# Performance work log

Hardware: AMD Instinct MI355X
Metric: run time of the kernel (lower is better)

Reference implementation:

```python
import jax, jax.numpy as jnp
import numpy as np

D_MODEL = 1024
NUM_HEADS = 16
HEAD_DIM = D_MODEL // NUM_HEADS
B, S = 4, 2048


def setup_inputs() -> dict:
    key = jax.random.key(0)
    ks = jax.random.split(key, 11)
    scale = 1.0 / np.sqrt(D_MODEL)
    return {
        "query": jax.random.normal(ks[0], (B, S, D_MODEL), jnp.float32),
        "key": jax.random.normal(ks[1], (B, S, D_MODEL), jnp.float32),
        "value": jax.random.normal(ks[2], (B, S, D_MODEL), jnp.float32),
        "Wq": jax.random.normal(ks[3], (D_MODEL, D_MODEL), jnp.float32) * scale,
        "bq": jnp.zeros((D_MODEL,), jnp.float32),
        "Wk": jax.random.normal(ks[4], (D_MODEL, D_MODEL), jnp.float32) * scale,
        "bk": jnp.zeros((D_MODEL,), jnp.float32),
        "Wv": jax.random.normal(ks[5], (D_MODEL, D_MODEL), jnp.float32) * scale,
        "bv": jnp.zeros((D_MODEL,), jnp.float32),
        "Wo": jax.random.normal(ks[6], (D_MODEL, D_MODEL), jnp.float32) * scale,
        "bo": jnp.zeros((D_MODEL,), jnp.float32),
    }


def reference(query, key, value, Wq, bq, Wk, bk, Wv, bv, Wo, bo):
    b = query.shape[0]
    # nn.Linear: x @ W.T + b; weights stored [out, in]
    def split_heads(x):
        return x.reshape(b, -1, NUM_HEADS, HEAD_DIM).transpose(0, 2, 1, 3)  # [b,h,s,d]
    q = split_heads(query @ Wq.T + bq)
    k = split_heads(key @ Wk.T + bk)
    v = split_heads(value @ Wv.T + bv)
    scores = jnp.einsum("bhqd,bhkd->bhqk", q, k) / np.sqrt(HEAD_DIM)
    weights = jax.nn.softmax(scores, axis=-1)
    out = jnp.einsum("bhqk,bhkd->bhqd", weights, v)
    out = out.transpose(0, 2, 1, 3).reshape(b, -1, D_MODEL)
    return out @ Wo.T + bo
```

## Files before the change

kernel.cpp:

```cpp
#include <hip/hip_runtime.h>

typedef __bf16 bf16;
typedef __bf16 bf16x4 __attribute__((ext_vector_type(4)));
typedef __bf16 bf16x8 __attribute__((ext_vector_type(8)));
typedef float f32x4 __attribute__((ext_vector_type(4)));

#define MFMA16(a, b, c) __builtin_amdgcn_mfma_f32_16x16x32_bf16((a), (b), (c), 0, 0, 0)

#define QSCALE 0.1803368808f

__device__ __forceinline__ void async_cp16(const bf16* g, bf16* l) {
    __builtin_amdgcn_global_load_lds((const __attribute__((address_space(1))) void*)g,
                                     (__attribute__((address_space(3))) void*)l, 16, 0, 0);
}

__global__ void cvt_bf16(const float* __restrict__ x, bf16* __restrict__ y, int n8) {
    int i = blockIdx.x * 256 + threadIdx.x;
    if (i >= n8) return;
    const float4* p = (const float4*)(x + (size_t)i * 8);
    float4 a = p[0], c = p[1];
    bf16x8 o;
    o[0] = (bf16)a.x; o[1] = (bf16)a.y; o[2] = (bf16)a.z; o[3] = (bf16)a.w;
    o[4] = (bf16)c.x; o[5] = (bf16)c.y; o[6] = (bf16)c.z; o[7] = (bf16)c.w;
    *(bf16x8*)(y + (size_t)i * 8) = o;
}

__device__ __forceinline__ void gemm_core(
    const bf16* __restrict__ A, const bf16* __restrict__ W,
    const float* __restrict__ bias, void* __restrict__ Cout,
    int mode, int m0, int n0)
{
    __shared__ bf16 As[128 * 32];
    __shared__ bf16 Bs[128 * 32];
    const int K = 1024;
    const int tid = threadIdx.x;
    const int lane = tid & 63, wave = tid >> 6;
    const int l15 = lane & 15, quad = lane >> 4;
    const int wm = wave >> 1, wn = wave & 1;

    f32x4 acc[4][4] = {};

    const int r0 = tid >> 2, k8 = (tid & 3) * 8;
    const bf16* Ag0 = A + (size_t)(m0 + r0) * K + k8;
    const bf16* Ag1 = A + (size_t)(m0 + r0 + 64) * K + k8;
    const bf16* Wg0 = W + (size_t)(n0 + r0) * K + k8;
    const bf16* Wg1 = W + (size_t)(n0 + r0 + 64) * K + k8;
    bf16* Al0 = As + tid * 8;
    bf16* Al1 = As + (tid + 256) * 8;
    bf16* Bl0 = Bs + tid * 8;
    bf16* Bl1 = Bs + (tid + 256) * 8;

    for (int k0 = 0; k0 < K; k0 += 32) {
        __syncthreads();
        async_cp16(Ag0 + k0, Al0);
        async_cp16(Ag1 + k0, Al1);
        async_cp16(Wg0 + k0, Bl0);
        async_cp16(Wg1 + k0, Bl1);
        __syncthreads();

        bf16x8 af[4], bfr[4];
#pragma unroll
        for (int t = 0; t < 4; ++t) {
            af[t]  = *(const bf16x8*)(As + (wm * 64 + t * 16 + l15) * 32 + quad * 8);
            bfr[t] = *(const bf16x8*)(Bs + (wn * 64 + t * 16 + l15) * 32 + quad * 8);
        }
#pragma unroll
        for (int mt = 0; mt < 4; ++mt)
#pragma unroll
            for (int nt = 0; nt < 4; ++nt)
                acc[mt][nt] = MFMA16(af[mt], bfr[nt], acc[mt][nt]);
    }

#pragma unroll
    for (int mt = 0; mt < 4; ++mt) {
#pragma unroll
        for (int nt = 0; nt < 4; ++nt) {
            int col = n0 + wn * 64 + nt * 16 + l15;
            float bcol = (mode == 2) ? 0.0f : bias[col];
#pragma unroll
            for (int r = 0; r < 4; ++r) {
                int row = m0 + wm * 64 + mt * 16 + quad * 4 + r;
                float val = acc[mt][nt][r];
                if (mode == 2) {
                    val += bias[row];
                    int bb = col >> 11, s = col & 2047;
                    int u = s & 63;
                    int sp = (s & ~63) | (((u & 15) << 2) | (u >> 4));
                    ((bf16*)Cout)[((size_t)(bb * 1024 + row) << 11) + sp] = (bf16)val;
                } else if (mode == 3) {
                    ((float*)Cout)[(size_t)row * 1024 + col] = val + bcol;
                } else {
                    val += bcol;
                    if (mode == 0) val *= QSCALE;
                    int bb = row >> 11, s = row & 2047, hh = col >> 6, d = col & 63;
                    ((bf16*)Cout)[(((size_t)(bb * 16 + hh) * 2048 + s) << 6) + d] = (bf16)val;
                }
            }
        }
    }
}

struct QkvArgs {
    const bf16* A[3];
    const bf16* W[3];
    const float* bias[3];
    bf16* out[3];
};

__global__ __launch_bounds__(256) void qkv_gemm(QkvArgs t) {
    int z = blockIdx.y;
    int bx = blockIdx.x;
    int m0, n0;
    if (z < 2) { m0 = (bx & 63) * 128; n0 = (bx >> 6) * 128; }
    else       { m0 = (bx & 7) * 128;  n0 = (bx >> 3) * 128; }
    gemm_core(t.A[z], t.W[z], t.bias[z], t.out[z], z, m0, n0);
}

__global__ __launch_bounds__(256) void oproj_gemm(
    const bf16* __restrict__ A, const bf16* __restrict__ W,
    const float* __restrict__ bias, float* __restrict__ Cout) {
    gemm_core(A, W, bias, Cout, 3, blockIdx.x * 128, blockIdx.y * 128);
}

__global__ __launch_bounds__(128, 2) void attn_kernel(
    const bf16* __restrict__ Qh, const bf16* __restrict__ Kh,
    const bf16* __restrict__ Vtg, bf16* __restrict__ AO)
{
    __shared__ bf16 Kl[64 * 64];
    __shared__ bf16 Vl[64 * 64];
    __shared__ bf16 Pl[2][64 * 72];

    const int tid = threadIdx.x;
    const int lane = tid & 63, wave = tid >> 6;
    const int l15 = lane & 15, quad = lane >> 4;
    const int l7 = l15 & 7;
    const int h = blockIdx.y, b = blockIdx.z;
    const int bh = b * 16 + h;
    const size_t base = (size_t)bh << 17;
    const int q0 = blockIdx.x * 128 + wave * 64;

    bf16x8 qf[4][2];
#pragma unroll
    for (int mt = 0; mt < 4; ++mt)
#pragma unroll
        for (int ks = 0; ks < 2; ++ks)
            qf[mt][ks] = *(const bf16x8*)(Qh + base + (q0 + mt * 16 + l15) * 64 + ks * 32 + quad * 8);

    f32x4 o[4][4] = {};
    float ls[4][4] = {};

    int srow[4], scol[4];
#pragma unroll
    for (int i = 0; i < 4; ++i) {
        int s = tid + i * 128;
        srow[i] = s >> 3;
        scol[i] = ((s & 7) ^ (srow[i] & 7)) * 8;
    }
    bf16* Pw = Pl[wave];

    for (int kt = 0; kt < 2048; kt += 64) {
        __syncthreads();
#pragma unroll
        for (int i = 0; i < 4; ++i) {
            int s = tid + i * 128;
            async_cp16(Kh + base + (size_t)(kt + srow[i]) * 64 + scol[i], Kl + s * 8);
            async_cp16(Vtg + base + (size_t)srow[i] * 2048 + kt + scol[i], Vl + s * 8);
        }
        __syncthreads();

        bf16x8 kb[2][4];
#pragma unroll
        for (int ks = 0; ks < 2; ++ks)
#pragma unroll
            for (int nt = 0; nt < 4; ++nt)
                kb[ks][nt] = *(const bf16x8*)(Kl + (nt * 16 + l15) * 64 + (((ks * 4 + quad) ^ l7) * 8));

#pragma unroll
        for (int mt = 0; mt < 4; ++mt) {
            f32x4 sc[4] = {};
#pragma unroll
            for (int ks = 0; ks < 2; ++ks)
#pragma unroll
                for (int nt = 0; nt < 4; ++nt)
                    sc[nt] = MFMA16(qf[mt][ks], kb[ks][nt], sc[nt]);
#pragma unroll
            for (int r = 0; r < 4; ++r) {
                float p0 = __builtin_amdgcn_exp2f(sc[0][r]);
                float p1 = __builtin_amdgcn_exp2f(sc[1][r]);
                float p2 = __builtin_amdgcn_exp2f(sc[2][r]);
                float p3 = __builtin_amdgcn_exp2f(sc[3][r]);
                ls[mt][r] += (p0 + p1) + (p2 + p3);
                bf16x4 pk = {(bf16)p0, (bf16)p1, (bf16)p2, (bf16)p3};
                *(bf16x4*)(Pw + (mt * 16 + quad * 4 + r) * 72 + l15 * 4) = pk;
            }
        }

        bf16x8 vb[2][4];
#pragma unroll
        for (int ks = 0; ks < 2; ++ks)
#pragma unroll
            for (int nt = 0; nt < 4; ++nt)
                vb[ks][nt] = *(const bf16x8*)(Vl + (nt * 16 + l15) * 64 + (((ks * 4 + quad) ^ l7) * 8));
#pragma unroll
        for (int mt = 0; mt < 4; ++mt)
#pragma unroll
            for (int ks = 0; ks < 2; ++ks) {
                bf16x8 pa = *(const bf16x8*)(Pw + (mt * 16 + l15) * 72 + ks * 32 + quad * 8);
#pragma unroll
                for (int nt = 0; nt < 4; ++nt)
                    o[mt][nt] = MFMA16(pa, vb[ks][nt], o[mt][nt]);
            }
    }

#pragma unroll
    for (int mt = 0; mt < 4; ++mt)
#pragma unroll
        for (int r = 0; r < 4; ++r) {
            float l = ls[mt][r];
            l += __shfl_xor(l, 1, 64);
            l += __shfl_xor(l, 2, 64);
            l += __shfl_xor(l, 4, 64);
            l += __shfl_xor(l, 8, 64);
            float inv = 1.0f / l;
            int s = q0 + mt * 16 + quad * 4 + r;
            size_t rowbase = ((size_t)(b * 2048 + s)) * 1024 + h * 64;
#pragma unroll
            for (int nt = 0; nt < 4; ++nt)
                AO[rowbase + nt * 16 + l15] = (bf16)(o[mt][nt][r] * inv);
        }
}

extern "C" void kernel_launch(void* const* d_in, const int* in_sizes, int n_in,
                              void* d_out, int out_size, void* d_ws, size_t ws_size,
                              hipStream_t stream) {
    const float* q  = (const float*)d_in[0];
    const float* k  = (const float*)d_in[1];
    const float* v  = (const float*)d_in[2];
    const float* Wq = (const float*)d_in[3];
    const float* bq = (const float*)d_in[4];
    const float* Wk = (const float*)d_in[5];
    const float* bk = (const float*)d_in[6];
    const float* Wv = (const float*)d_in[7];
    const float* bv = (const float*)d_in[8];
    const float* Wo = (const float*)d_in[9];
    const float* bo = (const float*)d_in[10];
    float* out = (float*)d_out;

    const size_t NX = (size_t)8192 * 1024;
    const size_t NW = (size_t)1024 * 1024;
    bf16* ws  = (bf16*)d_ws;
    bf16* Xq  = ws;
    bf16* Xk  = Xq + NX;
    bf16* Xv  = Xk + NX;
    bf16* Wqb = Xv + NX;
    bf16* Wkb = Wqb + NW;
    bf16* Wvb = Wkb + NW;
    bf16* Wob = Wvb + NW;
    bf16* Qh  = Wob + NW;
    bf16* Kh  = Qh + NX;
    bf16* Vt  = Kh + NX;
    bf16* AO  = Xq;

    int nx8 = (int)(NX / 8), nw8 = (int)(NW / 8);
    cvt_bf16<<<nx8 / 256, 256, 0, stream>>>(q, Xq, nx8);
    cvt_bf16<<<nx8 / 256, 256, 0, stream>>>(k, Xk, nx8);
    cvt_bf16<<<nx8 / 256, 256, 0, stream>>>(v, Xv, nx8);
    cvt_bf16<<<nw8 / 256, 256, 0, stream>>>(Wq, Wqb, nw8);
    cvt_bf16<<<nw8 / 256, 256, 0, stream>>>(Wk, Wkb, nw8);
    cvt_bf16<<<nw8 / 256, 256, 0, stream>>>(Wv, Wvb, nw8);
    cvt_bf16<<<nw8 / 256, 256, 0, stream>>>(Wo, Wob, nw8);

    dim3 bb(256, 1, 1);
    QkvArgs t;
    t.A[0] = Xq;  t.W[0] = Wqb; t.bias[0] = bq; t.out[0] = Qh;
    t.A[1] = Xk;  t.W[1] = Wkb; t.bias[1] = bk; t.out[1] = Kh;
    t.A[2] = Wvb; t.W[2] = Xv;  t.bias[2] = bv; t.out[2] = Vt;
    qkv_gemm<<<dim3(512, 3), bb, 0, stream>>>(t);

    attn_kernel<<<dim3(16, 16, 4), dim3(128, 1, 1), 0, stream>>>(Qh, Kh, Vt, AO);

    oproj_gemm<<<dim3(64, 8), bb, 0, stream>>>(AO, Wob, bo, out);
}
```

Baseline: 366.3 us.

## Keep attention probabilities in registers via transposed S and 16x16x16 MFMA

The attention kernel now computes S transposed (K as the A operand), so each lane's exp'd scores form a bf16x4 operand that feeds a 16x16x16 MFMA for the PV product directly. This removes the per-wave LDS round-trip for P and the shared memory it used. The block grows to 4 waves sharing each K/V tile, and the V layout permutation in the QKV epilogue is dropped. The seven fp32-to-bf16 conversion launches are merged into one kernel. The trade-off is twice as many smaller MFMA instructions for PV and higher register pressure from holding P.

Result: faster. 346.5 us (-5.4%).

```diff
diff --git a/kernel.cpp b/kernel.cpp
--- a/kernel.cpp
+++ b/kernel.cpp
@@ -3,9 +3,19 @@
 typedef __bf16 bf16;
 typedef __bf16 bf16x4 __attribute__((ext_vector_type(4)));
 typedef __bf16 bf16x8 __attribute__((ext_vector_type(8)));
+typedef short short4v __attribute__((ext_vector_type(4)));
 typedef float f32x4 __attribute__((ext_vector_type(4)));
 
 #define MFMA16(a, b, c) __builtin_amdgcn_mfma_f32_16x16x32_bf16((a), (b), (c), 0, 0, 0)
+
+__device__ __forceinline__ f32x4 mfma_16x16x16(bf16x4 a, bf16x4 b, f32x4 c) {
+#if __has_builtin(__builtin_amdgcn_mfma_f32_16x16x16_bf16)
+    return __builtin_amdgcn_mfma_f32_16x16x16_bf16(a, b, c, 0, 0, 0);
+#else
+    return __builtin_amdgcn_mfma_f32_16x16x16bf16_1k(
+        __builtin_bit_cast(short4v, a), __builtin_bit_cast(short4v, b), c, 0, 0, 0);
+#endif
+}
 
 #define QSCALE 0.1803368808f
 
@@ -14,15 +24,18 @@
                                      (__attribute__((address_space(3))) void*)l, 16, 0, 0);
 }
 
-__global__ void cvt_bf16(const float* __restrict__ x, bf16* __restrict__ y, int n8) {
-    int i = blockIdx.x * 256 + threadIdx.x;
-    if (i >= n8) return;
-    const float4* p = (const float4*)(x + (size_t)i * 8);
-    float4 a = p[0], c = p[1];
+struct CvtArgs { const float* src[7]; bf16* dst[7]; };
+__global__ void cvt_all(CvtArgs a) {
+    int bx = blockIdx.x, t, off;
+    if (bx < 12288) { t = bx >> 12;            off = bx & 4095; }
+    else            { t = 3 + ((bx - 12288) >> 9); off = (bx - 12288) & 511; }
+    size_t i = (size_t)off * 256 + threadIdx.x;
+    const float4* p = (const float4*)(a.src[t] + i * 8);
+    float4 x = p[0], y = p[1];
     bf16x8 o;
-    o[0] = (bf16)a.x; o[1] = (bf16)a.y; o[2] = (bf16)a.z; o[3] = (bf16)a.w;
-    o[4] = (bf16)c.x; o[5] = (bf16)c.y; o[6] = (bf16)c.z; o[7] = (bf16)c.w;
-    *(bf16x8*)(y + (size_t)i * 8) = o;
+    o[0] = (bf16)x.x; o[1] = (bf16)x.y; o[2] = (bf16)x.z; o[3] = (bf16)x.w;
+    o[4] = (bf16)y.x; o[5] = (bf16)y.y; o[6] = (bf16)y.z; o[7] = (bf16)y.w;
+    *(bf16x8*)(a.dst[t] + i * 8) = o;
 }
 
 __device__ __forceinline__ void gemm_core(
@@ -84,9 +97,7 @@
                 if (mode == 2) {
                     val += bias[row];
                     int bb = col >> 11, s = col & 2047;
-                    int u = s & 63;
-                    int sp = (s & ~63) | (((u & 15) << 2) | (u >> 4));
-                    ((bf16*)Cout)[((size_t)(bb * 1024 + row) << 11) + sp] = (bf16)val;
+                    ((bf16*)Cout)[((size_t)(bb * 1024 + row) << 11) + s] = (bf16)val;
                 } else if (mode == 3) {
                     ((float*)Cout)[(size_t)row * 1024 + col] = val + bcol;
                 } else {
@@ -122,112 +133,102 @@
     gemm_core(A, W, bias, Cout, 3, blockIdx.x * 128, blockIdx.y * 128);
 }
 
-__global__ __launch_bounds__(128, 2) void attn_kernel(
+__global__ __launch_bounds__(256, 2) void attn_kernel(
     const bf16* __restrict__ Qh, const bf16* __restrict__ Kh,
     const bf16* __restrict__ Vtg, bf16* __restrict__ AO)
 {
     __shared__ bf16 Kl[64 * 64];
     __shared__ bf16 Vl[64 * 64];
-    __shared__ bf16 Pl[2][64 * 72];
 
     const int tid = threadIdx.x;
     const int lane = tid & 63, wave = tid >> 6;
-    const int l15 = lane & 15, quad = lane >> 4;
-    const int l7 = l15 & 7;
+    const int l15 = lane & 15, quad = lane >> 4, l7 = l15 & 7;
     const int h = blockIdx.y, b = blockIdx.z;
-    const int bh = b * 16 + h;
-    const size_t base = (size_t)bh << 17;
-    const int q0 = blockIdx.x * 128 + wave * 64;
+    const size_t base = (size_t)(b * 16 + h) << 17;
+    const int q0 = blockIdx.x * 256 + wave * 64;
 
     bf16x8 qf[4][2];
 #pragma unroll
-    for (int mt = 0; mt < 4; ++mt)
+    for (int qt = 0; qt < 4; ++qt)
 #pragma unroll
         for (int ks = 0; ks < 2; ++ks)
-            qf[mt][ks] = *(const bf16x8*)(Qh + base + (q0 + mt * 16 + l15) * 64 + ks * 32 + quad * 8);
+            qf[qt][ks] = *(const bf16x8*)(Qh + base + (q0 + qt * 16 + l15) * 64 + ks * 32 + quad * 8);
 
     f32x4 o[4][4] = {};
-    float ls[4][4] = {};
-
-    int srow[4], scol[4];
-#pragma unroll
-    for (int i = 0; i < 4; ++i) {
-        int s = tid + i * 128;
-        srow[i] = s >> 3;
-        scol[i] = ((s & 7) ^ (srow[i] & 7)) * 8;
-    }
-    bf16* Pw = Pl[wave];
+    float ls[4] = {};
+
+    const int sr = tid >> 3;
+    const int sc0 = ((tid & 7) ^ (sr & 7)) * 8;
+    const int sr2 = sr + 32;
 
     for (int kt = 0; kt < 2048; kt += 64) {
         __syncthreads();
-#pragma unroll
-        for (int i = 0; i < 4; ++i) {
-            int s = tid + i * 128;
-            async_cp16(Kh + base + (size_t)(kt + srow[i]) * 64 + scol[i], Kl + s * 8);
-            async_cp16(Vtg + base + (size_t)srow[i] * 2048 + kt + scol[i], Vl + s * 8);
-        }
+        async_cp16(Kh + base + (size_t)(kt + sr) * 64 + sc0, Kl + tid * 8);
+        async_cp16(Kh + base + (size_t)(kt + sr2) * 64 + sc0, Kl + (tid + 256) * 8);
+        async_cp16(Vtg + base + (size_t)sr * 2048 + kt + sc0, Vl + tid * 8);
+        async_cp16(Vtg + base + (size_t)sr2 * 2048 + kt + sc0, Vl + (tid + 256) * 8);
         __syncthreads();
 
         bf16x8 kb[2][4];
 #pragma unroll
         for (int ks = 0; ks < 2; ++ks)
 #pragma unroll
-            for (int nt = 0; nt < 4; ++nt)
-                kb[ks][nt] = *(const bf16x8*)(Kl + (nt * 16 + l15) * 64 + (((ks * 4 + quad) ^ l7) * 8));
-
-#pragma unroll
-        for (int mt = 0; mt < 4; ++mt) {
+            for (int ktile = 0; ktile < 4; ++ktile)
+                kb[ks][ktile] = *(const bf16x8*)(Kl + (ktile * 16 + l15) * 64 + (((ks * 4 + quad) ^ l7) * 8));
+
+        bf16x4 pf[4][4];
+#pragma unroll
+        for (int qt = 0; qt < 4; ++qt) {
             f32x4 sc[4] = {};
 #pragma unroll
             for (int ks = 0; ks < 2; ++ks)
 #pragma unroll
-                for (int nt = 0; nt < 4; ++nt)
-                    sc[nt] = MFMA16(qf[mt][ks], kb[ks][nt], sc[nt]);
-#pragma unroll
-            for (int r = 0; r < 4; ++r) {
-                float p0 = __builtin_amdgcn_exp2f(sc[0][r]);
-                float p1 = __builtin_amdgcn_exp2f(sc[1][r]);
-                float p2 = __builtin_amdgcn_exp2f(sc[2][r]);
-                float p3 = __builtin_amdgcn_exp2f(sc[3][r]);
-                ls[mt][r] += (p0 + p1) + (p2 + p3);
-                bf16x4 pk = {(bf16)p0, (bf16)p1, (bf16)p2, (bf16)p3};
-                *(bf16x4*)(Pw + (mt * 16 + quad * 4 + r) * 72 + l15 * 4) = pk;
+                for (int ktile = 0; ktile < 4; ++ktile)
+                    sc[ktile] = MFMA16(kb[ks][ktile], qf[qt][ks], sc[ktile]);
+            float sum = 0.0f;
+#pragma unroll
+            for (int ktile = 0; ktile < 4; ++ktile) {
+                float p0 = __builtin_amdgcn_exp2f(sc[ktile][0]);
+                float p1 = __builtin_amdgcn_exp2f(sc[ktile][1]);
+                float p2 = __builtin_amdgcn_exp2f(sc[ktile][2]);
+                float p3 = __builtin_amdgcn_exp2f(sc[ktile][3]);
+                sum += (p0 + p1) + (p2 + p3);
+                pf[qt][ktile] = bf16x4{(bf16)p0, (bf16)p1, (bf16)p2, (bf16)p3};
             }
-        }
-
-        bf16x8 vb[2][4];
-#pragma unroll
-        for (int ks = 0; ks < 2; ++ks)
-#pragma unroll
-            for (int nt = 0; nt < 4; ++nt)
-                vb[ks][nt] = *(const bf16x8*)(Vl + (nt * 16 + l15) * 64 + (((ks * 4 + quad) ^ l7) * 8));
-#pragma unroll
-        for (int mt = 0; mt < 4; ++mt)
-#pragma unroll
-            for (int ks = 0; ks < 2; ++ks) {
-                bf16x8 pa = *(const bf16x8*)(Pw + (mt * 16 + l15) * 72 + ks * 32 + quad * 8);
-#pragma unroll
-                for (int nt = 0; nt < 4; ++nt)
-                    o[mt][nt] = MFMA16(pa, vb[ks][nt], o[mt][nt]);
-            }
-    }
-
-#pragma unroll
-    for (int mt = 0; mt < 4; ++mt)
-#pragma unroll
-        for (int r = 0; r < 4; ++r) {
-            float l = ls[mt][r];
-            l += __shfl_xor(l, 1, 64);
-            l += __shfl_xor(l, 2, 64);
-            l += __shfl_xor(l, 4, 64);
-            l += __shfl_xor(l, 8, 64);
-            float inv = 1.0f / l;
-            int s = q0 + mt * 16 + quad * 4 + r;
-            size_t rowbase = ((size_t)(b * 2048 + s)) * 1024 + h * 64;
-#pragma unroll
-            for (int nt = 0; nt < 4; ++nt)
-                AO[rowbase + nt * 16 + l15] = (bf16)(o[mt][nt][r] * inv);
-        }
+            ls[qt] += sum;
+        }
+
+        bf16x4 va[4][4];
+#pragma unroll
+        for (int dt = 0; dt < 4; ++dt)
+#pragma unroll
+            for (int ktile = 0; ktile < 4; ++ktile)
+                va[dt][ktile] = *(const bf16x4*)(Vl + (dt * 16 + l15) * 64 +
+                                 (((ktile * 2 + (quad >> 1)) ^ l7) * 8) + (quad & 1) * 4);
+
+#pragma unroll
+        for (int dt = 0; dt < 4; ++dt)
+#pragma unroll
+            for (int qt = 0; qt < 4; ++qt)
+#pragma unroll
+                for (int ktile = 0; ktile < 4; ++ktile)
+                    o[dt][qt] = mfma_16x16x16(va[dt][ktile], pf[qt][ktile], o[dt][qt]);
+    }
+
+#pragma unroll
+    for (int qt = 0; qt < 4; ++qt) {
+        float l = ls[qt];
+        l += __shfl_xor(l, 16, 64);
+        l += __shfl_xor(l, 32, 64);
+        float inv = 1.0f / l;
+        size_t rb = ((size_t)(b * 2048 + q0 + qt * 16 + l15)) * 1024 + h * 64;
+#pragma unroll
+        for (int dt = 0; dt < 4; ++dt) {
+            bf16x4 ov = {(bf16)(o[dt][qt][0] * inv), (bf16)(o[dt][qt][1] * inv),
+                         (bf16)(o[dt][qt][2] * inv), (bf16)(o[dt][qt][3] * inv)};
+            *(bf16x4*)(AO + rb + dt * 16 + quad * 4) = ov;
+        }
+    }
 }
 
 extern "C" void kernel_launch(void* const* d_in, const int* in_sizes, int n_in,
@@ -261,14 +262,15 @@
     bf16* Vt  = Kh + NX;
     bf16* AO  = Xq;
 
-    int nx8 = (int)(NX / 8), nw8 = (int)(NW / 8);
-    cvt_bf16<<<nx8 / 256, 256, 0, stream>>>(q, Xq, nx8);
-    cvt_bf16<<<nx8 / 256, 256, 0, stream>>>(k, Xk, nx8);
-    cvt_bf16<<<nx8 / 256, 256, 0, stream>>>(v, Xv, nx8);
-    cvt_bf16<<<nw8 / 256, 256, 0, stream>>>(Wq, Wqb, nw8);
-    cvt_bf16<<<nw8 / 256, 256, 0, stream>>>(Wk, Wkb, nw8);
-    cvt_bf16<<<nw8 / 256, 256, 0, stream>>>(Wv, Wvb, nw8);
-    cvt_bf16<<<nw8 / 256, 256, 0, stream>>>(Wo, Wob, nw8);
+    CvtArgs ca;
+    ca.src[0] = q;  ca.dst[0] = Xq;
+    ca.src[1] = k;  ca.dst[1] = Xk;
+    ca.src[2] = v;  ca.dst[2] = Xv;
+    ca.src[3] = Wq; ca.dst[3] = Wqb;
+    ca.src[4] = Wk; ca.dst[4] = Wkb;
+    ca.src[5] = Wv; ca.dst[5] = Wvb;
+    ca.src[6] = Wo; ca.dst[6] = Wob;
+    cvt_all<<<14336, 256, 0, stream>>>(ca);
 
     dim3 bb(256, 1, 1);
     QkvArgs t;
@@ -277,7 +279,7 @@
     t.A[2] = Wvb; t.W[2] = Xv;  t.bias[2] = bv; t.out[2] = Vt;
     qkv_gemm<<<dim3(512, 3), bb, 0, stream>>>(t);
 
-    attn_kernel<<<dim3(16, 16, 4), dim3(128, 1, 1), 0, stream>>>(Qh, Kh, Vt, AO);
+    attn_kernel<<<dim3(8, 16, 4), bb, 0, stream>>>(Qh, Kh, Vt, AO);
 
     oproj_gemm<<<dim3(64, 8), bb, 0, stream>>>(AO, Wob, bo, out);
 }
```
